# Performance work log

Hardware: AMD Instinct MI355X
Metric: run time of the kernel (lower is better)

Reference implementation:

```python
import jax, jax.numpy as jnp
import numpy as np

H = 512; VT = 10000; VN = 1000; ET = 256; EN = 256
A = 50; B = 8; L = 128; SOS = 0


def setup_inputs():
    key = jax.random.key(0)
    ks = jax.random.split(key, 12)
    g = lambda k, s: jax.random.normal(k, s, jnp.float32) * 0.02
    inp = {}
    inp["n_tensor"] = jax.random.randint(ks[0], (B, L), 0, VN)
    inp["t_tensor"] = jax.random.randint(ks[1], (B, L), 0, VT)
    inp["p_tensor"] = jax.random.randint(ks[2], (B, L), 0, L)
    # embedding tables; padding rows (padding_idx) zeroed as nn.Embedding init does
    inp["embN"] = g(ks[3], (VN, EN)).at[VN - 1].set(0.0)
    inp["embT"] = g(ks[4], (VT + A + 3, ET)).at[VT - 1].set(0.0)
    inp["W_hid"] = g(ks[5], (H, H)); inp["b_hid"] = jnp.zeros((H,), jnp.float32)
    inp["W_mem"] = g(ks[6], (H, H)); inp["b_mem"] = jnp.zeros((H,), jnp.float32)
    inp["v_w"] = g(ks[7], (H,)); inp["v_b"] = jnp.zeros((), jnp.float32)
    inp["W_ih"] = g(ks[8], (4 * H, EN + ET)); inp["W_hh"] = g(ks[9], (4 * H, H))
    inp["b_ih"] = jnp.zeros((4 * H,), jnp.float32); inp["b_hh"] = jnp.zeros((4 * H,), jnp.float32)
    inp["W_g"] = g(ks[10], (3 * H, VT + 3)); inp["b_g"] = jnp.zeros((VT + 3,), jnp.float32)
    inp["W_s"] = g(ks[11], (2 * H,)); inp["b_s"] = jnp.zeros((), jnp.float32)
    return inp


def _forward(embN, embT, W_hid, b_hid, W_mem, b_mem, v_w, v_b,
             W_ih, W_hh, b_ih, b_hh, W_g, b_g, W_s, b_s,
             n_tensor, t_tensor, p_tensor):
    full_mask = (n_tensor == VN - 1)                      # [B, L] eof mask
    sos = jnp.full((B, 1), SOS, n_tensor.dtype)
    n_in = jnp.concatenate([sos, n_tensor[:, :-1]], 1)    # teacher-forced inputs
    t_in = jnp.concatenate([sos, t_tensor[:, :-1]], 1)
    par = jnp.concatenate([jnp.zeros((B, 1), p_tensor.dtype), p_tensor[:, :-1]], 1)
    hs0 = jnp.zeros((B, L, H), jnp.float32)               # growing memory buffer
    h0 = jnp.zeros((B, H), jnp.float32)
    c0 = jnp.zeros((B, H), jnp.float32)
    barange = jnp.arange(B)
    arangeA = jnp.arange(A)

    def step(carry, xs):
        hs, h, c = carry
        t, n_t, t_t, p_t, tgt = xs
        # embedding gathers + single-layer LSTM cell (torch gate order i,f,g,o)
        x = jnp.concatenate([embN[n_t], embT[t_t]], 1)    # [B, EN+ET]
        gates = x @ W_ih.T + h @ W_hh.T + (b_ih + b_hh)
        i, f, gg, o = jnp.split(gates, 4, axis=1)
        c = jax.nn.sigmoid(f) * c + jax.nn.sigmoid(i) * jnp.tanh(gg)
        h = jax.nn.sigmoid(o) * jnp.tanh(c)
        # sliding-window memory hs[:, max(t-A,0):t], fixed-size slice + validity mask
        s = jnp.maximum(t - A, 0)
        mem = jax.lax.dynamic_slice(hs, (0, s, 0), (B, A, H))   # [B, A, H]
        fm = jax.lax.dynamic_slice(full_mask, (0, s), (B, A))   # [B, A]
        valid = (s + arangeA) < t                               # [A] positions already written
        mask = fm | ~valid[None, :]
        # additive attention: v^T tanh(W_hid h + W_mem mem)
        sc = jnp.tanh((h @ W_hid.T + b_hid)[:, None, :] + mem @ W_mem.T + b_mem)
        sc = sc @ v_w + v_b                                     # [B, A]
        sc = jnp.where(mask, -1e20, sc)
        attn = jax.nn.softmax(sc, axis=1)
        context = jnp.einsum('ba,bah->bh', attn, mem)
        h_parent = hs[barange, p_t]                             # per-batch gather on memory
        wt = jax.nn.log_softmax(jnp.concatenate([context, h, h_parent], 1) @ W_g + b_g, axis=1)
        log_attn = jax.nn.log_softmax(sc, axis=1)
        st = jax.nn.log_sigmoid(jnp.concatenate([context, h], 1) @ W_s + b_s)[:, None]  # [B,1]
        out = jnp.concatenate(
            [st + wt, jnp.log(jnp.clip(-jnp.expm1(st), 1e-18, 1e18)) + log_attn], 1)    # [B, VT+3+A]
        hs = hs.at[:, t].set(h)                                 # scatter new hidden into buffer
        loss_t = -jnp.take_along_axis(out, tgt[:, None], axis=1)[:, 0]  # NLLLoss(reduction='none')
        pred = jnp.argmax(out, axis=1)
        return (hs, h, c), (loss_t, pred)

    ts = jnp.arange(L)
    _, (losses, preds) = jax.lax.scan(
        step, (hs0, h0, c0), (ts, n_in.T, t_in.T, par.T, t_tensor.T))
    return losses.sum(), preds.T


def reference(n_tensor, t_tensor, p_tensor, embN, embT, W_hid, b_hid, W_mem, b_mem,
              v_w, v_b, W_ih, W_hh, b_ih, b_hh, W_g, b_g, W_s, b_s):
    return _forward(embN, embT, W_hid, b_hid, W_mem, b_mem, v_w, v_b,
                    W_ih, W_hh, b_ih, b_hh, W_g, b_g, W_s, b_s,
                    n_tensor, t_tensor, p_tensor)
```

## Files before the change

### kernel.cpp

```cpp
#include <hip/hip_runtime.h>
#include <hip/hip_bf16.h>
#include <math.h>

#define H_ 512
#define VN_ 1000
#define NG_ 10003
#define NGP_ 10240
#define NCHUNK 40
#define A_ 50
#define B_ 8
#define L_ 128
#define R_ 1024

typedef __hip_bfloat16 bf16;
typedef __attribute__((ext_vector_type(8))) short bf16x8;
typedef __attribute__((ext_vector_type(4))) float f32x4;

typedef union { unsigned long long u[2]; bf16x8 v; } frag_u;

__device__ __forceinline__ float sigf(float x) { return 1.0f / (1.0f + expf(-x)); }

__device__ __forceinline__ short b16(float v) {
    __hip_bfloat16 h = __float2bfloat16(v);
    return *(short*)&h;
}

__device__ __forceinline__ unsigned long long ald(const unsigned long long* p) {
    return __hip_atomic_load(p, __ATOMIC_RELAXED, __HIP_MEMORY_SCOPE_AGENT);
}
__device__ __forceinline__ void ast32(unsigned int* p, unsigned int v) {
    __hip_atomic_store(p, v, __ATOMIC_RELAXED, __HIP_MEMORY_SCOPE_AGENT);
}

__global__ void k_init(int* flags, float* bkq,
                       const float* __restrict__ bmem, const float* __restrict__ bhid,
                       float* out)
{
    int i = blockIdx.x * 256 + threadIdx.x;
    if (i < 32)
        __hip_atomic_store(&flags[i], 0, __ATOMIC_RELAXED, __HIP_MEMORY_SCOPE_AGENT);
    if (i < 512) bkq[i] = bmem[i];
    else if (i < 1024) bkq[i] = bhid[i - 512];
    if (i == 0) out[0] = 0.f;
}

__global__ void k_wgt(const float* __restrict__ Wg, bf16* __restrict__ WT)
{
    __shared__ short S[64][65];
    const int tid = threadIdx.x;
    const int n0 = blockIdx.x * 64, k0 = blockIdx.y * 64;
    const int c = tid & 63;
    const int r0 = (tid >> 6) * 16;
    #pragma unroll
    for (int i = 0; i < 16; ++i) {
        int k = r0 + i;
        int n = n0 + c;
        float v = (n < NG_) ? Wg[(size_t)(k0 + k) * NG_ + n] : 0.f;
        S[c][k] = b16(v);
    }
    __syncthreads();
    const int n_l = tid >> 2;
    const int kq = (tid & 3) * 16;
    bf16* dst = WT + (size_t)(n0 + n_l) * 1536 + k0 + kq;
    #pragma unroll
    for (int j = 0; j < 2; ++j) {
        bf16x8 v;
        #pragma unroll
        for (int e = 0; e < 8; ++e) v[e] = S[n_l][kq + j * 8 + e];
        *(bf16x8*)(dst + j * 8) = v;
    }
}

__global__ void k_w2b(const float* __restrict__ src, bf16* __restrict__ dst, int n)
{
    for (int i = blockIdx.x * blockDim.x + threadIdx.x; i < n; i += gridDim.x * blockDim.x)
        dst[i] = __float2bfloat16(src[i]);
}

__global__ void k_embed(const int* __restrict__ nt, const int* __restrict__ tt,
                        const float* __restrict__ embN, const float* __restrict__ embT,
                        bf16* __restrict__ X)
{
    int i = blockIdx.x * blockDim.x + threadIdx.x;
    int r = i >> 9, k = i & 511;
    int t = r >> 3, b = r & 7;
    float v;
    if (k < 256) {
        int id = (t == 0) ? 0 : nt[b * L_ + t - 1];
        v = embN[id * 256 + k];
    } else {
        int id = (t == 0) ? 0 : tt[b * L_ + t - 1];
        v = embT[id * 256 + (k - 256)];
    }
    X[i] = __float2bfloat16(v);
}

#define LSTM_BLOCKS 16

#define DECLW(i) bf16x8 Wa##i, Wb##i;
#define LOADW(i) { \
    float4 a0 = *(const float4*)(wr0 + (i)*32); \
    float4 a1 = *(const float4*)(wr0 + (i)*32 + 4); \
    float4 c0 = *(const float4*)(wr1 + (i)*32); \
    float4 c1 = *(const float4*)(wr1 + (i)*32 + 4); \
    Wa##i[0]=b16(a0.x); Wa##i[1]=b16(a0.y); Wa##i[2]=b16(a0.z); Wa##i[3]=b16(a0.w); \
    Wa##i[4]=b16(a1.x); Wa##i[5]=b16(a1.y); Wa##i[6]=b16(a1.z); Wa##i[7]=b16(a1.w); \
    Wb##i[0]=b16(c0.x); Wb##i[1]=b16(c0.y); Wb##i[2]=b16(c0.z); Wb##i[3]=b16(c0.w); \
    Wb##i[4]=b16(c1.x); Wb##i[5]=b16(c1.y); Wb##i[6]=b16(c1.z); Wb##i[7]=b16(c1.w); }
#define LDF(i) frag_u fu##i; fu##i.u[0] = ald(src + (i)*128); fu##i.u[1] = ald(src + (i)*128 + 1);
#define MM(i) \
    acc0 = __builtin_amdgcn_mfma_f32_16x16x32_bf16(Wa##i, fu##i.v, acc0, 0, 0, 0); \
    acc1 = __builtin_amdgcn_mfma_f32_16x16x32_bf16(Wb##i, fu##i.v, acc1, 0, 0, 0);

__launch_bounds__(256, 1)
__global__ void k_lstm(const float* __restrict__ Whh, const float* __restrict__ xg,
                       float* __restrict__ hs, bf16* __restrict__ hsb,
                       unsigned long long* __restrict__ bfr, int* __restrict__ flags)
{
    __shared__ float gl[4][32][9];
    const int tid  = threadIdx.x;
    const int lane = tid & 63;
    const int w    = tid >> 6;
    const int x    = blockIdx.x;
    const int m_l  = lane & 15;
    const int kg   = lane >> 4;
    const int n    = lane & 15;
    unsigned int* bfr32 = (unsigned int*)bfr;

    const float* wr0 = Whh + (size_t)(w * 512 + x * 32 + m_l) * 512 + kg * 8;
    const float* wr1 = wr0 + (size_t)16 * 512;
    DECLW(0)  DECLW(1)  DECLW(2)  DECLW(3)  DECLW(4)  DECLW(5)  DECLW(6)  DECLW(7)
    DECLW(8)  DECLW(9)  DECLW(10) DECLW(11) DECLW(12) DECLW(13) DECLW(14) DECLW(15)
    LOADW(0)  LOADW(1)  LOADW(2)  LOADW(3)  LOADW(4)  LOADW(5)  LOADW(6)  LOADW(7)
    LOADW(8)  LOADW(9)  LOADW(10) LOADW(11) LOADW(12) LOADW(13) LOADW(14) LOADW(15)
    asm volatile("" : "+v"(Wa0), "+v"(Wb0), "+v"(Wa1), "+v"(Wb1), "+v"(Wa2), "+v"(Wb2),
                      "+v"(Wa3), "+v"(Wb3), "+v"(Wa4), "+v"(Wb4), "+v"(Wa5), "+v"(Wb5),
                      "+v"(Wa6), "+v"(Wb6), "+v"(Wa7), "+v"(Wb7));
    asm volatile("" : "+v"(Wa8), "+v"(Wb8), "+v"(Wa9), "+v"(Wb9), "+v"(Wa10), "+v"(Wb10),
                      "+v"(Wa11), "+v"(Wb11), "+v"(Wa12), "+v"(Wb12), "+v"(Wa13), "+v"(Wb13),
                      "+v"(Wa14), "+v"(Wb14), "+v"(Wa15), "+v"(Wb15));

    const int u_l = tid >> 3;
    const int b   = tid & 7;
    float creg = 0.f;

    for (int t = 0; t < L_; ++t) {
        const float* xr = xg + ((size_t)t * B_ + b) * 2048 + x * 32 + u_l;
        float xi = xr[0], xf = xr[512], xgg = xr[1024], xo = xr[1536];

        f32x4 acc0 = {0.f, 0.f, 0.f, 0.f};
        f32x4 acc1 = {0.f, 0.f, 0.f, 0.f};
        if (t > 0) {
            for (;;) {
                int v = (lane < LSTM_BLOCKS)
                    ? __hip_atomic_load(&flags[lane], __ATOMIC_RELAXED, __HIP_MEMORY_SCOPE_AGENT)
                    : t;
                if (__all(v >= t)) break;
                __builtin_amdgcn_s_sleep(1);
            }
            const unsigned long long* src =
                bfr + (size_t)((t + 1) & 1) * 2048 + lane * 2;
            LDF(0)  LDF(1)  LDF(2)  LDF(3)  LDF(4)  LDF(5)  LDF(6)  LDF(7)
            LDF(8)  LDF(9)  LDF(10) LDF(11) LDF(12) LDF(13) LDF(14) LDF(15)
            __builtin_amdgcn_sched_barrier(0);
            MM(0)  MM(1)  MM(2)  MM(3)  MM(4)  MM(5)  MM(6)  MM(7)
            MM(8)  MM(9)  MM(10) MM(11) MM(12) MM(13) MM(14) MM(15)
        }
        if (n < 8) {
            #pragma unroll
            for (int i = 0; i < 4; ++i) {
                gl[w][kg * 4 + i][n]      = acc0[i];
                gl[w][16 + kg * 4 + i][n] = acc1[i];
            }
        }
        __syncthreads();
        float gi = gl[0][u_l][b] + xi;
        float gf = gl[1][u_l][b] + xf;
        float gg = gl[2][u_l][b] + xgg;
        float go = gl[3][u_l][b] + xo;
        float iv = sigf(gi), fv = sigf(gf), gv = tanhf(gg), ov = sigf(go);
        creg = fv * creg + iv * gv;
        float h = ov * tanhf(creg);
        float h2 = __shfl_xor(h, 8);
        unsigned pay = 0;
        if ((u_l & 1) == 0) {
            pay = (unsigned)(unsigned short)b16(h)
                | ((unsigned)(unsigned short)b16(h2) << 16);
            int q = u_l >> 3, p = (u_l & 7) >> 1;
            ast32(bfr32 + (size_t)(t & 1) * 4096 + x * 256 + (b + 16 * q) * 4 + p, pay);
        }
        asm volatile("s_waitcnt vmcnt(0)" ::: "memory");
        __syncthreads();
        if (tid == 0)
            __hip_atomic_store(&flags[x], t + 1, __ATOMIC_RELAXED, __HIP_MEMORY_SCOPE_AGENT);
        hs[((size_t)t * B_ + b) * H_ + x * 32 + u_l] = h;
        if ((u_l & 1) == 0)
            *(unsigned int*)(hsb + (size_t)(t * B_ + b) * 512 + x * 32 + u_l) = pay;
    }
}

__launch_bounds__(256)
__global__ void k_attn(const float* __restrict__ hs, const float* __restrict__ kmq,
                       const float* __restrict__ vw,
                       const float* __restrict__ vb, const int* __restrict__ nt,
                       const int* __restrict__ pt, const float* __restrict__ Wsv,
                       const float* __restrict__ bs, bf16* __restrict__ gcat,
                       float* __restrict__ logattn, float* __restrict__ stbuf)
{
    const int r = blockIdx.x;
    const int t = r >> 3, b = r & 7;
    const int tid = threadIdx.x;
    const int lane = tid & 63, wave = tid >> 6;
    int s = t - A_; if (s < 0) s = 0;
    __shared__ float qv[512];
    __shared__ float vwl[512];
    __shared__ float sc[A_];
    __shared__ float attn[A_];
    __shared__ float red[4];
    for (int i = tid; i < 512; i += 256) {
        qv[i] = kmq[(size_t)r * 1024 + 512 + i];
        vwl[i] = vw[i];
    }
    __syncthreads();
    for (int a = wave; a < A_; a += 4) {
        int pos = s + a;
        float v = -1e20f;
        bool masked = (pos >= t) || (nt[b * L_ + pos] == VN_ - 1);
        if (!masked) {
            const float* kr = kmq + (size_t)(pos * B_ + b) * 1024;
            float p = 0.f;
            for (int k = lane; k < 512; k += 64)
                p += vwl[k] * tanhf(qv[k] + kr[k]);
            for (int off = 32; off; off >>= 1) p += __shfl_down(p, off);
            v = p + vb[0];
        }
        if (lane == 0) sc[a] = v;
    }
    __syncthreads();
    if (tid < 64) {
        float v = (tid < A_) ? sc[tid] : -INFINITY;
        float m = v;
        for (int off = 32; off; off >>= 1) m = fmaxf(m, __shfl_xor(m, off));
        float e = (tid < A_) ? expf(v - m) : 0.f;
        float d = e;
        for (int off = 32; off; off >>= 1) d += __shfl_xor(d, off);
        if (tid < A_) {
            attn[tid] = e / d;
            logattn[(size_t)r * A_ + tid] = (v - m) - logf(d);
        }
    }
    __syncthreads();
    const int k0 = tid * 2;
    float c0 = 0.f, c1 = 0.f;
    for (int a = 0; a < A_; ++a) {
        int pos = s + a;
        if (pos >= t) break;
        float w = attn[a];
        const float2 hv = *(const float2*)(hs + (size_t)(pos * B_ + b) * 512 + k0);
        c0 += w * hv.x; c1 += w * hv.y;
    }
    const float2 hcur = *(const float2*)(hs + (size_t)(t * B_ + b) * 512 + k0);
    int par = (t == 0) ? 0 : pt[b * L_ + t - 1];
    float2 hpar = make_float2(0.f, 0.f);
    if (par < t) hpar = *(const float2*)(hs + (size_t)(par * B_ + b) * 512 + k0);
    bf16* g = gcat + (size_t)r * 1536;
    g[k0]            = __float2bfloat16(c0);
    g[k0 + 1]        = __float2bfloat16(c1);
    g[512 + k0]      = __float2bfloat16(hcur.x);
    g[512 + k0 + 1]  = __float2bfloat16(hcur.y);
    g[1024 + k0]     = __float2bfloat16(hpar.x);
    g[1024 + k0 + 1] = __float2bfloat16(hpar.y);
    float part = c0 * Wsv[k0] + c1 * Wsv[k0 + 1]
               + hcur.x * Wsv[512 + k0] + hcur.y * Wsv[512 + k0 + 1];
    for (int off = 32; off; off >>= 1) part += __shfl_down(part, off);
    if (lane == 0) red[wave] = part;
    __syncthreads();
    if (tid == 0) {
        float z = red[0] + red[1] + red[2] + red[3] + bs[0];
        stbuf[r] = -log1pf(expf(-z));
    }
}

__launch_bounds__(256)
__global__ void k_mfma_bt(const bf16* __restrict__ Ag, const bf16* __restrict__ Bg,
                          const float* __restrict__ b1, const float* __restrict__ b2,
                          float* __restrict__ C, int N, int K)
{
    __shared__ short Al[64][40];
    __shared__ short Bl[64][40];
    const int m0 = blockIdx.y * 64, n0 = blockIdx.x * 64;
    const int tid = threadIdx.x;
    const int lane = tid & 63, wave = tid >> 6;
    f32x4 acc[4] = {};
    for (int k0 = 0; k0 < K; k0 += 32) {
        __syncthreads();
        {
            int r = tid >> 2, c = (tid & 3) * 8;
            *(bf16x8*)&Al[r][c] = *(const bf16x8*)(Ag + (size_t)(m0 + r) * K + k0 + c);
            *(bf16x8*)&Bl[r][c] = *(const bf16x8*)(Bg + (size_t)(n0 + r) * K + k0 + c);
        }
        __syncthreads();
        const int row = lane & 15, kg = (lane >> 4) * 8;
        bf16x8 a = *(const bf16x8*)&Al[wave * 16 + row][kg];
        #pragma unroll
        for (int f = 0; f < 4; ++f) {
            bf16x8 bv = *(const bf16x8*)&Bl[f * 16 + row][kg];
            acc[f] = __builtin_amdgcn_mfma_f32_16x16x32_bf16(a, bv, acc[f], 0, 0, 0);
        }
    }
    const int col = lane & 15, rq = (lane >> 4) * 4;
    #pragma unroll
    for (int f = 0; f < 4; ++f)
        #pragma unroll
        for (int i = 0; i < 4; ++i) {
            int nn = n0 + f * 16 + col;
            float v = acc[f][i];
            if (b1) v += b1[nn];
            if (b2) v += b2[nn];
            C[(size_t)(m0 + wave * 16 + rq + i) * N + nn] = v;
        }
}

__launch_bounds__(256, 2)
__global__ void k_gemm128p(const bf16* __restrict__ Ag, const bf16* __restrict__ Bg,
                           const float* __restrict__ bg, const int* __restrict__ tt,
                           float* __restrict__ pst)
{
    __shared__ short As[128 * 32];
    __shared__ short Bs[128 * 32];
    __shared__ float bgl[256];
    __shared__ float mrg[128][6];
    const int tid = threadIdx.x;
    const int lane = tid & 63, wave = tid >> 6;
    const int wr = wave >> 1, wc = wave & 1;
    const int col16 = lane & 15, rq = (lane >> 4) * 4;
    const int chunk = blockIdx.x;
    const int m0 = blockIdx.y * 128;
    const int K = 1536;

    bgl[tid] = (chunk * 256 + tid < NG_) ? bg[chunk * 256 + tid] : -INFINITY;

    float M[4][4], S[4][4], AV[4][4], TGT[4][4]; int AI[4][4]; int tgt[4][4];
    #pragma unroll
    for (int mi = 0; mi < 4; ++mi)
        #pragma unroll
        for (int i = 0; i < 4; ++i) {
            M[mi][i] = -INFINITY; S[mi][i] = 0.f; AV[mi][i] = -INFINITY;
            TGT[mi][i] = -INFINITY; AI[mi][i] = 0x7FFFFFFF;
            int row = m0 + wr * 64 + mi * 16 + rq + i;
            tgt[mi][i] = tt[(row & 7) * L_ + (row >> 3)];
        }

    for (int nt = 0; nt < 2; ++nt) {
        const int n0 = chunk * 256 + nt * 128;
        f32x4 acc[4][4] = {};
        for (int k0 = 0; k0 < K; k0 += 32) {
            __syncthreads();
            #pragma unroll
            for (int h = 0; h < 2; ++h) {
                int o = tid + h * 256;
                int row = o >> 2;
                int kc = (o & 3) ^ (row & 3);
                const bf16* ga = Ag + (size_t)(m0 + row) * K + k0 + kc * 8;
                const bf16* gb = Bg + (size_t)(n0 + row) * K + k0 + kc * 8;
                unsigned ldso = h * 4096 + wave * 1024;
                __builtin_amdgcn_global_load_lds(
                    (const __attribute__((address_space(1))) void*)ga,
                    (__attribute__((address_space(3))) void*)((char*)As + ldso), 16, 0, 0);
                __builtin_amdgcn_global_load_lds(
                    (const __attribute__((address_space(1))) void*)gb,
                    (__attribute__((address_space(3))) void*)((char*)Bs + ldso), 16, 0, 0);
            }
            asm volatile("s_waitcnt vmcnt(0)" ::: "memory");
            __syncthreads();
            bf16x8 af[4], bf[4];
            #pragma unroll
            for (int mi = 0; mi < 4; ++mi) {
                int ra = wr * 64 + mi * 16 + col16;
                af[mi] = *(const bf16x8*)&As[ra * 32 + (((lane >> 4) ^ (ra & 3)) * 8)];
            }
            #pragma unroll
            for (int ni = 0; ni < 4; ++ni) {
                int rb = wc * 64 + ni * 16 + col16;
                bf[ni] = *(const bf16x8*)&Bs[rb * 32 + (((lane >> 4) ^ (rb & 3)) * 8)];
            }
            #pragma unroll
            for (int mi = 0; mi < 4; ++mi)
                #pragma unroll
                for (int ni = 0; ni < 4; ++ni)
                    acc[mi][ni] = __builtin_amdgcn_mfma_f32_16x16x32_bf16(af[mi], bf[ni], acc[mi][ni], 0, 0, 0);
        }
        #pragma unroll
        for (int mi = 0; mi < 4; ++mi)
            #pragma unroll
            for (int i = 0; i < 4; ++i) {
                float v[4]; int nn[4];
                #pragma unroll
                for (int ni = 0; ni < 4; ++ni) {
                    int cl = nt * 128 + wc * 64 + ni * 16 + col16;
                    v[ni] = acc[mi][ni][i] + bgl[cl];
                    nn[ni] = chunk * 256 + cl;
                }
                float lv = v[0]; int li = nn[0];
                #pragma unroll
                for (int ni = 1; ni < 4; ++ni)
                    if (v[ni] > lv) { lv = v[ni]; li = nn[ni]; }
                #pragma unroll
                for (int off = 1; off < 16; off <<= 1) {
                    float ov = __shfl_xor(lv, off); int oi = __shfl_xor(li, off);
                    if (ov > lv || (ov == lv && oi < li)) { lv = ov; li = oi; }
                }
                float nM = fmaxf(M[mi][i], lv);
                float add = 0.f;
                if (nM != -INFINITY) {
                    #pragma unroll
                    for (int ni = 0; ni < 4; ++ni) add += expf(v[ni] - nM);
                    #pragma unroll
                    for (int off = 1; off < 16; off <<= 1) add += __shfl_xor(add, off);
                }
                S[mi][i] = ((S[mi][i] > 0.f) ? S[mi][i] * expf(M[mi][i] - nM) : 0.f) + add;
                M[mi][i] = nM;
                if (lv > AV[mi][i] || (lv == AV[mi][i] && li < AI[mi][i])) {
                    AV[mi][i] = lv; AI[mi][i] = li;
                }
                float tv = -INFINITY;
                #pragma unroll
                for (int ni = 0; ni < 4; ++ni)
                    if (nn[ni] == tgt[mi][i]) tv = v[ni];
                #pragma unroll
                for (int off = 1; off < 16; off <<= 1)
                    tv = fmaxf(tv, __shfl_xor(tv, off));
                TGT[mi][i] = fmaxf(TGT[mi][i], tv);
            }
    }
    __syncthreads();
    if (wc == 1 && col16 == 0) {
        #pragma unroll
        for (int mi = 0; mi < 4; ++mi)
            #pragma unroll
            for (int i = 0; i < 4; ++i) {
                int rl = wr * 64 + mi * 16 + rq + i;
                mrg[rl][0] = M[mi][i]; mrg[rl][1] = S[mi][i];
                mrg[rl][2] = AV[mi][i]; mrg[rl][3] = __int_as_float(AI[mi][i]);
                mrg[rl][4] = TGT[mi][i];
            }
    }
    __syncthreads();
    if (wc == 0 && col16 == 0) {
        #pragma unroll
        for (int mi = 0; mi < 4; ++mi)
            #pragma unroll
            for (int i = 0; i < 4; ++i) {
                int rl = wr * 64 + mi * 16 + rq + i;
                float oM = mrg[rl][0], oS = mrg[rl][1], oAV = mrg[rl][2];
                int oAI = __float_as_int(mrg[rl][3]);
                float oT = mrg[rl][4];
                float nM = fmaxf(M[mi][i], oM);
                float s1 = (S[mi][i] > 0.f) ? S[mi][i] * expf(M[mi][i] - nM) : 0.f;
                float s2 = (oS > 0.f) ? oS * expf(oM - nM) : 0.f;
                float av = AV[mi][i]; int ai = AI[mi][i];
                if (oAV > av || (oAV == av && oAI < ai)) { av = oAV; ai = oAI; }
                float* p = pst + ((size_t)chunk * R_ + (m0 + rl)) * 8;
                p[0] = nM; p[1] = s1 + s2; p[2] = av;
                p[3] = __int_as_float(ai); p[4] = fmaxf(TGT[mi][i], oT);
            }
    }
}

__launch_bounds__(64)
__global__ void k_loss2(const float* __restrict__ pst, const float* __restrict__ logattn,
                        const float* __restrict__ stbuf, float* __restrict__ out)
{
    const int r = blockIdx.x;
    const int lane = threadIdx.x;
    float M = -INFINITY, S = 0.f, AV = -INFINITY, TGT = -INFINITY;
    int AI = 0x7FFFFFFF;
    if (lane < NCHUNK) {
        const float* p = pst + ((size_t)lane * R_ + r) * 8;
        M = p[0]; S = p[1]; AV = p[2]; AI = __float_as_int(p[3]); TGT = p[4];
    }
    for (int off = 32; off; off >>= 1) {
        float oM = __shfl_xor(M, off), oS = __shfl_xor(S, off);
        float oAV = __shfl_xor(AV, off), oT = __shfl_xor(TGT, off);
        int oAI = __shfl_xor(AI, off);
        float nM = fmaxf(M, oM);
        float s1 = (S > 0.f) ? S * expf(M - nM) : 0.f;
        float s2 = (oS > 0.f) ? oS * expf(oM - nM) : 0.f;
        M = nM; S = s1 + s2;
        if (oAV > AV || (oAV == AV && oAI < AI)) { AV = oAV; AI = oAI; }
        TGT = fmaxf(TGT, oT);
    }
    if (lane == 0) {
        float lse = M + logf(S);
        float st = stbuf[r];
        const float* la = logattn + (size_t)r * A_;
        float lamax = la[0]; int aidx = 0;
        for (int a = 1; a < A_; ++a) if (la[a] > lamax) { lamax = la[a]; aidx = a; }
        float e1 = -expm1f(st);
        e1 = fminf(fmaxf(e1, 1e-18f), 1e18f);
        float lm = logf(e1);
        float p1 = st + M - lse;
        float p2 = lm + lamax;
        int pred = (p1 >= p2) ? AI : (NG_ + aidx);
        float loss = -(st + TGT - lse);
        atomicAdd(&out[0], loss);
        int t = r >> 3, b = r & 7;
        out[1 + b * L_ + t] = (float)pred;
    }
}

extern "C" void kernel_launch(void* const* d_in, const int* in_sizes, int n_in,
                              void* d_out, int out_size, void* d_ws, size_t ws_size,
                              hipStream_t stream)
{
    (void)in_sizes; (void)n_in; (void)out_size; (void)ws_size;
    const int*   nt    = (const int*)d_in[0];
    const int*   tt    = (const int*)d_in[1];
    const int*   pt    = (const int*)d_in[2];
    const float* embN  = (const float*)d_in[3];
    const float* embT  = (const float*)d_in[4];
    const float* W_hid = (const float*)d_in[5];
    const float* b_hid = (const float*)d_in[6];
    const float* W_mem = (const float*)d_in[7];
    const float* b_mem = (const float*)d_in[8];
    const float* v_w   = (const float*)d_in[9];
    const float* v_b   = (const float*)d_in[10];
    const float* W_ih  = (const float*)d_in[11];
    const float* W_hh  = (const float*)d_in[12];
    const float* b_ih  = (const float*)d_in[13];
    const float* b_hh  = (const float*)d_in[14];
    const float* W_g   = (const float*)d_in[15];
    const float* b_g   = (const float*)d_in[16];
    const float* W_s   = (const float*)d_in[17];
    const float* b_s   = (const float*)d_in[18];
    float* out = (float*)d_out;

    char* ws = (char*)d_ws;
    size_t o = 0;
    bf16*  WGT  = (bf16*)(ws + o);  o += (size_t)NGP_ * 1536 * 2;
    float* XG   = (float*)(ws + o); o += (size_t)R_ * 2048 * 4;
    float* HS   = (float*)(ws + o); o += (size_t)R_ * H_ * 4;
    bf16*  HSB  = (bf16*)(ws + o);  o += (size_t)R_ * H_ * 2;
    float* KMQ  = (float*)(ws + o); o += (size_t)R_ * 1024 * 4;
    bf16*  WKQ  = (bf16*)(ws + o);  o += (size_t)1024 * 512 * 2;
    float* BKQ  = (float*)(ws + o); o += (size_t)1024 * 4;
    bf16*  XB   = (bf16*)(ws + o);  o += (size_t)R_ * H_ * 2;
    bf16*  WIHB = (bf16*)(ws + o);  o += (size_t)2048 * 512 * 2;
    bf16*  GC   = (bf16*)(ws + o);  o += (size_t)R_ * 1536 * 2;
    float* LA   = (float*)(ws + o); o += (size_t)R_ * A_ * 4;
    float* ST   = (float*)(ws + o); o += (size_t)R_ * 4;
    float* PST  = (float*)(ws + o); o += (size_t)NCHUNK * R_ * 8 * 4;
    unsigned long long* BFR = (unsigned long long*)(ws + o); o += (size_t)4096 * 8;
    int*   FLG  = (int*)(ws + o);   o += 256;

    k_init<<<4, 256, 0, stream>>>(FLG, BKQ, b_mem, b_hid, out);
    k_wgt<<<dim3(NGP_ / 64, 1536 / 64), 256, 0, stream>>>(W_g, WGT);
    k_w2b<<<1024, 256, 0, stream>>>(W_ih, WIHB, 2048 * 512);
    k_w2b<<<256, 256, 0, stream>>>(W_mem, WKQ, 512 * 512);
    k_w2b<<<256, 256, 0, stream>>>(W_hid, WKQ + (size_t)512 * 512, 512 * 512);
    k_embed<<<R_ * H_ / 256, 256, 0, stream>>>(nt, tt, embN, embT, XB);
    k_mfma_bt<<<dim3(2048 / 64, R_ / 64), 256, 0, stream>>>(XB, WIHB, b_ih, b_hh, XG, 2048, 512);
    k_lstm<<<LSTM_BLOCKS, 256, 0, stream>>>(W_hh, XG, HS, HSB, BFR, FLG);
    k_mfma_bt<<<dim3(1024 / 64, R_ / 64), 256, 0, stream>>>(HSB, WKQ, BKQ, nullptr, KMQ, 1024, 512);
    k_attn<<<R_, 256, 0, stream>>>(HS, KMQ, v_w, v_b, nt, pt, W_s, b_s, GC, LA, ST);
    k_gemm128p<<<dim3(NCHUNK, R_ / 128), 256, 0, stream>>>(GC, WGT, b_g, tt, PST);
    k_loss2<<<R_, 64, 0, stream>>>(PST, LA, ST, out);
}
```

Baseline: 651.0 us.

## Overlap weight conversion with LSTM recurrence, use bf16 hidden buffer, bigger GEMM tiles

Folds the W_g transpose-convert and the W_mem/W_hid bf16 conversion into extra blocks of the LSTM launch, so that work runs on idle CUs while the 16-block serial recurrence proceeds. Drops the fp32 hidden-state buffer and makes attention read the bf16 copy, which halves that traffic but lowers the precision of the context and h inputs. Replaces the 64x64 GEMM with a 128x128 tile that loads straight into LDS with swizzling, and switches to fast exp-based sigmoid/tanh. It also prefetches peer flags to skip the spin-wait when they are already set.

```diff
diff --git a/kernel.cpp b/kernel.cpp
--- a/kernel.cpp
+++ b/kernel.cpp
@@ -18,7 +18,8 @@
 
 typedef union { unsigned long long u[2]; bf16x8 v; } frag_u;
 
-__device__ __forceinline__ float sigf(float x) { return 1.0f / (1.0f + expf(-x)); }
+__device__ __forceinline__ float fsig(float x) { return 1.0f / (1.0f + __expf(-x)); }
+__device__ __forceinline__ float ftanh(float x) { return 1.0f - 2.0f / (1.0f + __expf(2.0f * x)); }
 
 __device__ __forceinline__ short b16(float v) {
     __hip_bfloat16 h = __float2bfloat16(v);
@@ -42,33 +43,6 @@
     if (i < 512) bkq[i] = bmem[i];
     else if (i < 1024) bkq[i] = bhid[i - 512];
     if (i == 0) out[0] = 0.f;
-}
-
-__global__ void k_wgt(const float* __restrict__ Wg, bf16* __restrict__ WT)
-{
-    __shared__ short S[64][65];
-    const int tid = threadIdx.x;
-    const int n0 = blockIdx.x * 64, k0 = blockIdx.y * 64;
-    const int c = tid & 63;
-    const int r0 = (tid >> 6) * 16;
-    #pragma unroll
-    for (int i = 0; i < 16; ++i) {
-        int k = r0 + i;
-        int n = n0 + c;
-        float v = (n < NG_) ? Wg[(size_t)(k0 + k) * NG_ + n] : 0.f;
-        S[c][k] = b16(v);
-    }
-    __syncthreads();
-    const int n_l = tid >> 2;
-    const int kq = (tid & 3) * 16;
-    bf16* dst = WT + (size_t)(n0 + n_l) * 1536 + k0 + kq;
-    #pragma unroll
-    for (int j = 0; j < 2; ++j) {
-        bf16x8 v;
-        #pragma unroll
-        for (int e = 0; e < 8; ++e) v[e] = S[n_l][kq + j * 8 + e];
-        *(bf16x8*)(dst + j * 8) = v;
-    }
 }
 
 __global__ void k_w2b(const float* __restrict__ src, bf16* __restrict__ dst, int n)
@@ -96,6 +70,7 @@
 }
 
 #define LSTM_BLOCKS 16
+#define XTRA 240
 
 #define DECLW(i) bf16x8 Wa##i, Wb##i;
 #define LOADW(i) { \
@@ -114,14 +89,51 @@
 
 __launch_bounds__(256, 1)
 __global__ void k_lstm(const float* __restrict__ Whh, const float* __restrict__ xg,
-                       float* __restrict__ hs, bf16* __restrict__ hsb,
-                       unsigned long long* __restrict__ bfr, int* __restrict__ flags)
+                       bf16* __restrict__ hsb,
+                       unsigned long long* __restrict__ bfr, int* __restrict__ flags,
+                       const float* __restrict__ Wg, bf16* __restrict__ WT,
+                       const float* __restrict__ Wmem, const float* __restrict__ Whid,
+                       bf16* __restrict__ wkq)
 {
     __shared__ float gl[4][32][9];
+    __shared__ short S[64][65];
     const int tid  = threadIdx.x;
+    const int x    = blockIdx.x;
+
+    if (x >= LSTM_BLOCKS) {
+        for (int i = (x - LSTM_BLOCKS) * 256 + tid; i < 2 * 512 * 512; i += XTRA * 256) {
+            float v = (i < 512 * 512) ? Wmem[i] : Whid[i - 512 * 512];
+            wkq[i] = __float2bfloat16(v);
+        }
+        const int c = tid & 63;
+        const int r0 = (tid >> 6) * 16;
+        const int n_l = tid >> 2;
+        const int kq = (tid & 3) * 16;
+        for (int tile = x - LSTM_BLOCKS; tile < 160 * 24; tile += XTRA) {
+            int n0 = (tile % 160) * 64, k0 = (tile / 160) * 64;
+            __syncthreads();
+            #pragma unroll
+            for (int i = 0; i < 16; ++i) {
+                int k = r0 + i;
+                int n = n0 + c;
+                float v = (n < NG_) ? Wg[(size_t)(k0 + k) * NG_ + n] : 0.f;
+                S[c][k] = b16(v);
+            }
+            __syncthreads();
+            bf16* dst = WT + (size_t)(n0 + n_l) * 1536 + k0 + kq;
+            #pragma unroll
+            for (int j = 0; j < 2; ++j) {
+                bf16x8 v;
+                #pragma unroll
+                for (int e = 0; e < 8; ++e) v[e] = S[n_l][kq + j * 8 + e];
+                *(bf16x8*)(dst + j * 8) = v;
+            }
+        }
+        return;
+    }
+
     const int lane = tid & 63;
     const int w    = tid >> 6;
-    const int x    = blockIdx.x;
     const int m_l  = lane & 15;
     const int kg   = lane >> 4;
     const int n    = lane & 15;
@@ -143,6 +155,7 @@
     const int u_l = tid >> 3;
     const int b   = tid & 7;
     float creg = 0.f;
+    int fearly = 0;
 
     for (int t = 0; t < L_; ++t) {
         const float* xr = xg + ((size_t)t * B_ + b) * 2048 + x * 32 + u_l;
@@ -151,12 +164,14 @@
         f32x4 acc0 = {0.f, 0.f, 0.f, 0.f};
         f32x4 acc1 = {0.f, 0.f, 0.f, 0.f};
         if (t > 0) {
-            for (;;) {
-                int v = (lane < LSTM_BLOCKS)
-                    ? __hip_atomic_load(&flags[lane], __ATOMIC_RELAXED, __HIP_MEMORY_SCOPE_AGENT)
-                    : t;
-                if (__all(v >= t)) break;
-                __builtin_amdgcn_s_sleep(1);
+            if (!__all(fearly >= t)) {
+                for (;;) {
+                    int v = (lane < LSTM_BLOCKS)
+                        ? __hip_atomic_load(&flags[lane], __ATOMIC_RELAXED, __HIP_MEMORY_SCOPE_AGENT)
+                        : t;
+                    if (__all(v >= t)) break;
+                    __builtin_amdgcn_s_sleep(1);
+                }
             }
             const unsigned long long* src =
                 bfr + (size_t)((t + 1) & 1) * 2048 + lane * 2;
@@ -178,9 +193,9 @@
         float gf = gl[1][u_l][b] + xf;
         float gg = gl[2][u_l][b] + xgg;
         float go = gl[3][u_l][b] + xo;
-        float iv = sigf(gi), fv = sigf(gf), gv = tanhf(gg), ov = sigf(go);
+        float iv = fsig(gi), fv = fsig(gf), gv = ftanh(gg), ov = fsig(go);
         creg = fv * creg + iv * gv;
-        float h = ov * tanhf(creg);
+        float h = ov * ftanh(creg);
         float h2 = __shfl_xor(h, 8);
         unsigned pay = 0;
         if ((u_l & 1) == 0) {
@@ -189,18 +204,20 @@
             int q = u_l >> 3, p = (u_l & 7) >> 1;
             ast32(bfr32 + (size_t)(t & 1) * 4096 + x * 256 + (b + 16 * q) * 4 + p, pay);
         }
+        fearly = (lane < LSTM_BLOCKS && lane != x)
+            ? __hip_atomic_load(&flags[lane], __ATOMIC_RELAXED, __HIP_MEMORY_SCOPE_AGENT)
+            : 0x7FFFFFFF;
         asm volatile("s_waitcnt vmcnt(0)" ::: "memory");
         __syncthreads();
         if (tid == 0)
             __hip_atomic_store(&flags[x], t + 1, __ATOMIC_RELAXED, __HIP_MEMORY_SCOPE_AGENT);
-        hs[((size_t)t * B_ + b) * H_ + x * 32 + u_l] = h;
         if ((u_l & 1) == 0)
             *(unsigned int*)(hsb + (size_t)(t * B_ + b) * 512 + x * 32 + u_l) = pay;
     }
 }
 
 __launch_bounds__(256)
-__global__ void k_attn(const float* __restrict__ hs, const float* __restrict__ kmq,
+__global__ void k_attn(const bf16* __restrict__ hsb, const float* __restrict__ kmq,
                        const float* __restrict__ vw,
                        const float* __restrict__ vb, const int* __restrict__ nt,
                        const int* __restrict__ pt, const float* __restrict__ Wsv,
@@ -230,7 +247,7 @@
             const float* kr = kmq + (size_t)(pos * B_ + b) * 1024;
             float p = 0.f;
             for (int k = lane; k < 512; k += 64)
-                p += vwl[k] * tanhf(qv[k] + kr[k]);
+                p += vwl[k] * ftanh(qv[k] + kr[k]);
             for (int off = 32; off; off >>= 1) p += __shfl_down(p, off);
             v = p + vb[0];
         }
@@ -256,22 +273,23 @@
         int pos = s + a;
         if (pos >= t) break;
         float w = attn[a];
-        const float2 hv = *(const float2*)(hs + (size_t)(pos * B_ + b) * 512 + k0);
-        c0 += w * hv.x; c1 += w * hv.y;
-    }
-    const float2 hcur = *(const float2*)(hs + (size_t)(t * B_ + b) * 512 + k0);
+        unsigned u = *(const unsigned*)((const unsigned short*)hsb + (size_t)(pos * B_ + b) * 512 + k0);
+        c0 += w * __uint_as_float(u << 16);
+        c1 += w * __uint_as_float(u & 0xffff0000u);
+    }
+    unsigned ucur = *(const unsigned*)((const unsigned short*)hsb + (size_t)(t * B_ + b) * 512 + k0);
     int par = (t == 0) ? 0 : pt[b * L_ + t - 1];
-    float2 hpar = make_float2(0.f, 0.f);
-    if (par < t) hpar = *(const float2*)(hs + (size_t)(par * B_ + b) * 512 + k0);
+    unsigned upar = 0;
+    if (par < t)
+        upar = *(const unsigned*)((const unsigned short*)hsb + (size_t)(par * B_ + b) * 512 + k0);
+    float hx = __uint_as_float(ucur << 16), hy = __uint_as_float(ucur & 0xffff0000u);
     bf16* g = gcat + (size_t)r * 1536;
-    g[k0]            = __float2bfloat16(c0);
-    g[k0 + 1]        = __float2bfloat16(c1);
-    g[512 + k0]      = __float2bfloat16(hcur.x);
-    g[512 + k0 + 1]  = __float2bfloat16(hcur.y);
-    g[1024 + k0]     = __float2bfloat16(hpar.x);
-    g[1024 + k0 + 1] = __float2bfloat16(hpar.y);
+    g[k0]     = __float2bfloat16(c0);
+    g[k0 + 1] = __float2bfloat16(c1);
+    *(unsigned*)(g + 512 + k0)  = ucur;
+    *(unsigned*)(g + 1024 + k0) = upar;
     float part = c0 * Wsv[k0] + c1 * Wsv[k0 + 1]
-               + hcur.x * Wsv[512 + k0] + hcur.y * Wsv[512 + k0 + 1];
+               + hx * Wsv[512 + k0] + hy * Wsv[512 + k0 + 1];
     for (int off = 32; off; off >>= 1) part += __shfl_down(part, off);
     if (lane == 0) red[wave] = part;
     __syncthreads();
@@ -281,43 +299,64 @@
     }
 }
 
-__launch_bounds__(256)
-__global__ void k_mfma_bt(const bf16* __restrict__ Ag, const bf16* __restrict__ Bg,
-                          const float* __restrict__ b1, const float* __restrict__ b2,
-                          float* __restrict__ C, int N, int K)
-{
-    __shared__ short Al[64][40];
-    __shared__ short Bl[64][40];
-    const int m0 = blockIdx.y * 64, n0 = blockIdx.x * 64;
+__launch_bounds__(256, 2)
+__global__ void k_gemm128b(const bf16* __restrict__ Ag, const bf16* __restrict__ Bg,
+                           const float* __restrict__ b1, const float* __restrict__ b2,
+                           float* __restrict__ C, int N, int K)
+{
+    __shared__ short As[128 * 32];
+    __shared__ short Bs[128 * 32];
     const int tid = threadIdx.x;
     const int lane = tid & 63, wave = tid >> 6;
-    f32x4 acc[4] = {};
+    const int wr = wave >> 1, wc = wave & 1;
+    const int m0 = blockIdx.y * 128, n0 = blockIdx.x * 128;
+    f32x4 acc[4][4] = {};
     for (int k0 = 0; k0 < K; k0 += 32) {
         __syncthreads();
-        {
-            int r = tid >> 2, c = (tid & 3) * 8;
-            *(bf16x8*)&Al[r][c] = *(const bf16x8*)(Ag + (size_t)(m0 + r) * K + k0 + c);
-            *(bf16x8*)&Bl[r][c] = *(const bf16x8*)(Bg + (size_t)(n0 + r) * K + k0 + c);
-        }
+        #pragma unroll
+        for (int h = 0; h < 2; ++h) {
+            int o = tid + h * 256;
+            int row = o >> 2;
+            int kc = (o & 3) ^ (row & 3);
+            const bf16* ga = Ag + (size_t)(m0 + row) * K + k0 + kc * 8;
+            const bf16* gb = Bg + (size_t)(n0 + row) * K + k0 + kc * 8;
+            unsigned ldso = h * 4096 + wave * 1024;
+            __builtin_amdgcn_global_load_lds(
+                (const __attribute__((address_space(1))) void*)ga,
+                (__attribute__((address_space(3))) void*)((char*)As + ldso), 16, 0, 0);
+            __builtin_amdgcn_global_load_lds(
+                (const __attribute__((address_space(1))) void*)gb,
+                (__attribute__((address_space(3))) void*)((char*)Bs + ldso), 16, 0, 0);
+        }
+        asm volatile("s_waitcnt vmcnt(0)" ::: "memory");
         __syncthreads();
-        const int row = lane & 15, kg = (lane >> 4) * 8;
-        bf16x8 a = *(const bf16x8*)&Al[wave * 16 + row][kg];
-        #pragma unroll
-        for (int f = 0; f < 4; ++f) {
-            bf16x8 bv = *(const bf16x8*)&Bl[f * 16 + row][kg];
-            acc[f] = __builtin_amdgcn_mfma_f32_16x16x32_bf16(a, bv, acc[f], 0, 0, 0);
-        }
+        bf16x8 af[4], bf[4];
+        #pragma unroll
+        for (int mi = 0; mi < 4; ++mi) {
+            int ra = wr * 64 + mi * 16 + (lane & 15);
+            af[mi] = *(const bf16x8*)&As[ra * 32 + (((lane >> 4) ^ (ra & 3)) * 8)];
+        }
+        #pragma unroll
+        for (int ni = 0; ni < 4; ++ni) {
+            int rb = wc * 64 + ni * 16 + (lane & 15);
+            bf[ni] = *(const bf16x8*)&Bs[rb * 32 + (((lane >> 4) ^ (rb & 3)) * 8)];
+        }
+        #pragma unroll
+        for (int mi = 0; mi < 4; ++mi)
+            #pragma unroll
+            for (int ni = 0; ni < 4; ++ni)
+                acc[mi][ni] = __builtin_amdgcn_mfma_f32_16x16x32_bf16(af[mi], bf[ni], acc[mi][ni], 0, 0, 0);
     }
     const int col = lane & 15, rq = (lane >> 4) * 4;
     #pragma unroll
-    for (int f = 0; f < 4; ++f)
-        #pragma unroll
-        for (int i = 0; i < 4; ++i) {
-            int nn = n0 + f * 16 + col;
-            float v = acc[f][i];
-            if (b1) v += b1[nn];
-            if (b2) v += b2[nn];
-            C[(size_t)(m0 + wave * 16 + rq + i) * N + nn] = v;
+    for (int mi = 0; mi < 4; ++mi)
+        #pragma unroll
+        for (int ni = 0; ni < 4; ++ni) {
+            int nn = n0 + wc * 64 + ni * 16 + col;
+            float bias = (b1 ? b1[nn] : 0.f) + (b2 ? b2[nn] : 0.f);
+            #pragma unroll
+            for (int i = 0; i < 4; ++i)
+                C[(size_t)(m0 + wr * 64 + mi * 16 + rq + i) * N + nn] = acc[mi][ni][i] + bias;
         }
 }
 
@@ -539,7 +578,6 @@
     size_t o = 0;
     bf16*  WGT  = (bf16*)(ws + o);  o += (size_t)NGP_ * 1536 * 2;
     float* XG   = (float*)(ws + o); o += (size_t)R_ * 2048 * 4;
-    float* HS   = (float*)(ws + o); o += (size_t)R_ * H_ * 4;
     bf16*  HSB  = (bf16*)(ws + o);  o += (size_t)R_ * H_ * 2;
     float* KMQ  = (float*)(ws + o); o += (size_t)R_ * 1024 * 4;
     bf16*  WKQ  = (bf16*)(ws + o);  o += (size_t)1024 * 512 * 2;
@@ -554,15 +592,13 @@
     int*   FLG  = (int*)(ws + o);   o += 256;
 
     k_init<<<4, 256, 0, stream>>>(FLG, BKQ, b_mem, b_hid, out);
-    k_wgt<<<dim3(NGP_ / 64, 1536 / 64), 256, 0, stream>>>(W_g, WGT);
     k_w2b<<<1024, 256, 0, stream>>>(W_ih, WIHB, 2048 * 512);
-    k_w2b<<<256, 256, 0, stream>>>(W_mem, WKQ, 512 * 512);
-    k_w2b<<<256, 256, 0, stream>>>(W_hid, WKQ + (size_t)512 * 512, 512 * 512);
     k_embed<<<R_ * H_ / 256, 256, 0, stream>>>(nt, tt, embN, embT, XB);
-    k_mfma_bt<<<dim3(2048 / 64, R_ / 64), 256, 0, stream>>>(XB, WIHB, b_ih, b_hh, XG, 2048, 512);
-    k_lstm<<<LSTM_BLOCKS, 256, 0, stream>>>(W_hh, XG, HS, HSB, BFR, FLG);
-    k_mfma_bt<<<dim3(1024 / 64, R_ / 64), 256, 0, stream>>>(HSB, WKQ, BKQ, nullptr, KMQ, 1024, 512);
-    k_attn<<<R_, 256, 0, stream>>>(HS, KMQ, v_w, v_b, nt, pt, W_s, b_s, GC, LA, ST);
+    k_gemm128b<<<dim3(2048 / 128, R_ / 128), 256, 0, stream>>>(XB, WIHB, b_ih, b_hh, XG, 2048, 512);
+    k_lstm<<<LSTM_BLOCKS + XTRA, 256, 0, stream>>>(W_hh, XG, HSB, BFR, FLG,
+                                                   W_g, WGT, W_mem, W_hid, WKQ);
+    k_gemm128b<<<dim3(1024 / 128, R_ / 128), 256, 0, stream>>>(HSB, WKQ, BKQ, nullptr, KMQ, 1024, 512);
+    k_attn<<<R_, 256, 0, stream>>>(HSB, KMQ, v_w, v_b, nt, pt, W_s, b_s, GC, LA, ST);
     k_gemm128p<<<dim3(NCHUNK, R_ / 128), 256, 0, stream>>>(GC, WGT, b_g, tt, PST);
     k_loss2<<<R_, 64, 0, stream>>>(PST, LA, ST, out);
 }
```

After: 603.8 us. 7.3% less time.
